# Performance work log

Measured on AMD Instinct MI355X. Metric: run time of the kernel, lower is better.

Reference implementation:

```python
import jax, jax.numpy as jnp
import numpy as np

NF = 128
NH = 512


def setup_inputs() -> dict:
    key = jax.random.key(0)
    k_x, k_wx, k_wh = jax.random.split(key, 3)
    B, T = 4096, 64
    x = jax.random.normal(k_x, (B, T, NF), dtype=jnp.float32)
    # GlorotUniform init: limit = sqrt(6 / (fan_in + fan_out))
    lim_x = float(np.sqrt(6.0 / (NF + NH)))
    lim_h = float(np.sqrt(6.0 / (NH + NH)))
    wx = jax.random.uniform(k_wx, (NF, NH), minval=-lim_x, maxval=lim_x, dtype=jnp.float32)
    wh = jax.random.uniform(k_wh, (NH, NH), minval=-lim_h, maxval=lim_h, dtype=jnp.float32)
    b = jnp.zeros((1, NH), dtype=jnp.float32)
    return {"x": x, "wx": wx, "wh": wh, "b": b}


def reference(x, wx, wh, b):
    # x: [B, T, nf] -> final hidden state [B, nh]
    B = x.shape[0]
    # Precompute input projections for all timesteps in one big GEMM: [T, B, nh]
    xz = jnp.einsum('btf,fh->tbh', x, wx) + b

    def step(h, xz_t):
        h = jnp.tanh(xz_t + h @ wh)
        return h, None

    h0 = jnp.zeros((B, wh.shape[0]), dtype=x.dtype)
    h_final, _ = jax.lax.scan(step, h0, xz)
    return h_final
```

## Files before the change

kernel.cpp:

```cpp
#include <hip/hip_runtime.h>
#include <math.h>


#define T_STEPS 64
#define NFD     128
#define NHD     512
#define BR      16
#define THREADS 1024
#define LDH     (NHD + 8)
#define LDX     (NFD + 8)

typedef _Float16 half8 __attribute__((ext_vector_type(8)));
typedef _Float16 half2v __attribute__((ext_vector_type(2)));
typedef float float4v __attribute__((ext_vector_type(4)));

__global__ __launch_bounds__(256) void rnn_prep(
    const float* __restrict__ wh, const float* __restrict__ wx,
    _Float16* __restrict__ whp_hi, _Float16* __restrict__ whp_lo,
    _Float16* __restrict__ wxp_hi, _Float16* __restrict__ wxp_lo)
{
    int idx = blockIdx.x * 256 + threadIdx.x;
    {
        int j  = idx & 7;
        int l  = (idx >> 3) & 63;
        int nt = (idx >> 9) & 3;
        int kb = (idx >> 11) & 15;
        int w  = idx >> 15;
        int k  = kb * 32 + (l >> 4) * 8 + j;
        int n  = w * 64 + nt * 16 + (l & 15);
        float v = wh[k * NHD + n];
        _Float16 hi = (_Float16)v;
        whp_hi[idx] = hi;
        whp_lo[idx] = (_Float16)(v - (float)hi);
    }
    if (idx < 65536) {
        int j  = idx & 7;
        int l  = (idx >> 3) & 63;
        int nt = (idx >> 9) & 3;
        int kb = (idx >> 11) & 3;
        int w  = idx >> 13;
        int k  = kb * 32 + (l >> 4) * 8 + j;
        int n  = w * 64 + nt * 16 + (l & 15);
        float v = wx[k * NHD + n];
        _Float16 hi = (_Float16)v;
        wxp_hi[idx] = hi;
        wxp_lo[idx] = (_Float16)(v - (float)hi);
    }
}

__device__ __forceinline__ float fast_tanh(float v) {
    float xc = fminf(fmaxf(v, -9.0f), 9.0f);
    float e  = __builtin_amdgcn_exp2f(xc * 2.8853900817779268f);
    return (e - 1.0f) * __builtin_amdgcn_rcpf(e + 1.0f);
}

__global__ __launch_bounds__(THREADS, 4) void rnn_mfma(
    const float* __restrict__ x,
    const float* __restrict__ bias,
    const _Float16* __restrict__ whp_hi, const _Float16* __restrict__ whp_lo,
    const _Float16* __restrict__ wxp_hi, const _Float16* __restrict__ wxp_lo,
    float* __restrict__ out)
{
    __shared__ _Float16 sh_hhi[BR * LDH];
    __shared__ _Float16 sh_hlo[BR * LDH];
    __shared__ _Float16 sh_xhi[BR * LDX];
    __shared__ _Float16 sh_xlo[BR * LDX];

    const int tid  = (int)threadIdx.x;
    const int lane = tid & 63;
    const int w    = tid >> 6;
    const int m    = lane & 15;
    const int quad = lane >> 4;
    const int row0 = (int)blockIdx.x * BR;

    for (int i = tid; i < BR * LDH; i += THREADS) {
        sh_hhi[i] = (_Float16)0.f;
        sh_hlo[i] = (_Float16)0.f;
    }

    float bv[2];
    #pragma unroll
    for (int nt = 0; nt < 2; ++nt) bv[nt] = bias[w * 32 + nt * 16 + m];

    const int xrow = tid >> 6;
    const int xcol = (tid & 63) * 2;
    const float* xptr = x + (size_t)(row0 + xrow) * (T_STEPS * NFD) + xcol;
    float2 px = *(const float2*)xptr;

    const half8* wxh = (const half8*)wxp_hi + (size_t)(w >> 1) * 1024 + (w & 1) * 128;
    const half8* wxl = (const half8*)wxp_lo + (size_t)(w >> 1) * 1024 + (w & 1) * 128;
    const half8* whh = (const half8*)whp_hi + (size_t)(w >> 1) * 4096 + (w & 1) * 128;
    const half8* whl = (const half8*)whp_lo + (size_t)(w >> 1) * 4096 + (w & 1) * 128;

    for (int t = 0; t < T_STEPS; ++t) {
        {
            half2v vh, vl;
            float xs[2] = {px.x, px.y};
            #pragma unroll
            for (int j = 0; j < 2; ++j) {
                _Float16 hi = (_Float16)xs[j];
                vh[j] = hi;
                vl[j] = (_Float16)(xs[j] - (float)hi);
            }
            *(half2v*)&sh_xhi[xrow * LDX + xcol] = vh;
            *(half2v*)&sh_xlo[xrow * LDX + xcol] = vl;
        }
        __syncthreads();

        if (t + 1 < T_STEPS) px = *(const float2*)(xptr + (t + 1) * NFD);

        float4v acc[2];
        #pragma unroll
        for (int nt = 0; nt < 2; ++nt) {
            acc[nt][0] = bv[nt]; acc[nt][1] = bv[nt];
            acc[nt][2] = bv[nt]; acc[nt][3] = bv[nt];
        }

        #pragma unroll
        for (int kb = 0; kb < 4; ++kb) {
            half8 ah = *(const half8*)&sh_xhi[m * LDX + kb * 32 + quad * 8];
            half8 al = *(const half8*)&sh_xlo[m * LDX + kb * 32 + quad * 8];
            half8 bh0 = wxh[kb * 256 + lane];
            half8 bh1 = wxh[kb * 256 + 64 + lane];
            half8 bl0 = wxl[kb * 256 + lane];
            half8 bl1 = wxl[kb * 256 + 64 + lane];
            acc[0] = __builtin_amdgcn_mfma_f32_16x16x32_f16(ah, bh0, acc[0], 0, 0, 0);
            acc[0] = __builtin_amdgcn_mfma_f32_16x16x32_f16(al, bh0, acc[0], 0, 0, 0);
            acc[0] = __builtin_amdgcn_mfma_f32_16x16x32_f16(ah, bl0, acc[0], 0, 0, 0);
            acc[1] = __builtin_amdgcn_mfma_f32_16x16x32_f16(ah, bh1, acc[1], 0, 0, 0);
            acc[1] = __builtin_amdgcn_mfma_f32_16x16x32_f16(al, bh1, acc[1], 0, 0, 0);
            acc[1] = __builtin_amdgcn_mfma_f32_16x16x32_f16(ah, bl1, acc[1], 0, 0, 0);
        }

        #pragma unroll 4
        for (int kb = 0; kb < 16; ++kb) {
            half8 ah = *(const half8*)&sh_hhi[m * LDH + kb * 32 + quad * 8];
            half8 al = *(const half8*)&sh_hlo[m * LDH + kb * 32 + quad * 8];
            half8 bh0 = whh[kb * 256 + lane];
            half8 bh1 = whh[kb * 256 + 64 + lane];
            half8 bl0 = whl[kb * 256 + lane];
            half8 bl1 = whl[kb * 256 + 64 + lane];
            acc[0] = __builtin_amdgcn_mfma_f32_16x16x32_f16(ah, bh0, acc[0], 0, 0, 0);
            acc[0] = __builtin_amdgcn_mfma_f32_16x16x32_f16(al, bh0, acc[0], 0, 0, 0);
            acc[0] = __builtin_amdgcn_mfma_f32_16x16x32_f16(ah, bl0, acc[0], 0, 0, 0);
            acc[1] = __builtin_amdgcn_mfma_f32_16x16x32_f16(ah, bh1, acc[1], 0, 0, 0);
            acc[1] = __builtin_amdgcn_mfma_f32_16x16x32_f16(al, bh1, acc[1], 0, 0, 0);
            acc[1] = __builtin_amdgcn_mfma_f32_16x16x32_f16(ah, bl1, acc[1], 0, 0, 0);
        }

        __syncthreads();

        if (t == T_STEPS - 1) {
            #pragma unroll
            for (int nt = 0; nt < 2; ++nt)
                #pragma unroll
                for (int r = 0; r < 4; ++r)
                    out[(size_t)(row0 + quad * 4 + r) * NHD + w * 32 + nt * 16 + m] =
                        fast_tanh(acc[nt][r]);
        } else {
            #pragma unroll
            for (int nt = 0; nt < 2; ++nt) {
                #pragma unroll
                for (int r = 0; r < 4; ++r) {
                    float v = fast_tanh(acc[nt][r]);
                    _Float16 hi = (_Float16)v;
                    int off = (quad * 4 + r) * LDH + w * 32 + nt * 16 + m;
                    sh_hhi[off] = hi;
                    sh_hlo[off] = (_Float16)(v - (float)hi);
                }
            }
        }
    }
}

extern "C" void kernel_launch(void* const* d_in, const int* in_sizes, int n_in,
                              void* d_out, int out_size, void* d_ws, size_t ws_size,
                              hipStream_t stream) {
    const float* x    = (const float*)d_in[0];
    const float* wx   = (const float*)d_in[1];
    const float* wh   = (const float*)d_in[2];
    const float* bias = (const float*)d_in[3];
    float* out = (float*)d_out;

    char* ws = (char*)d_ws;
    _Float16* whp_hi = (_Float16*)(ws);
    _Float16* whp_lo = (_Float16*)(ws + 524288);
    _Float16* wxp_hi = (_Float16*)(ws + 1048576);
    _Float16* wxp_lo = (_Float16*)(ws + 1048576 + 131072);

    rnn_prep<<<1024, 256, 0, stream>>>(wh, wx, whp_hi, whp_lo, wxp_hi, wxp_lo);

    const int B = in_sizes[0] / (T_STEPS * NFD);
    rnn_mfma<<<B / BR, THREADS, 0, stream>>>(x, bias, whp_hi, whp_lo, wxp_hi, wxp_lo, out);
}
```

Before: 843.5 us.

## Split hidden dimension across block pairs with global-memory h exchange and flags

Each 32-row batch tile is now handled by two cooperating blocks, each computing half of the hidden columns. The blocks swap their half of h through double-buffered global memory and spin on per-pair flags. The aim is to halve each block's Wh traffic per row and to overlap the own-half matmul with waiting for the partner. The risk is a deadlock if both partner blocks are not resident at the same time, since grid size is 256 blocks of 1024 threads. The per-step global round-trip and spin-wait also add latency, and a fallback path keeps the old kernel when the workspace is too small.

```diff
diff --git a/kernel.cpp b/kernel.cpp
--- a/kernel.cpp
+++ b/kernel.cpp
@@ -5,16 +5,238 @@
 #define T_STEPS 64
 #define NFD     128
 #define NHD     512
-#define BR      16
 #define THREADS 1024
-#define LDH     (NHD + 8)
 #define LDX     (NFD + 8)
 
 typedef _Float16 half8 __attribute__((ext_vector_type(8)));
+typedef _Float16 half4v __attribute__((ext_vector_type(4)));
 typedef _Float16 half2v __attribute__((ext_vector_type(2)));
 typedef float float4v __attribute__((ext_vector_type(4)));
 
+#define OFF_WHH   0u
+#define OFF_WHL   (512u<<10)
+#define OFF_WXH   (1024u<<10)
+#define OFF_WXL   (1152u<<10)
+#define OFF_FLAGS (1280u<<10)
+#define OFF_XH    (2048u<<10)
+#define OFF_XL    (10240u<<10)
+#define WS_NEED   (18432u<<10)
+
+__device__ __forceinline__ float fast_tanh(float v) {
+    float xc = fminf(fmaxf(v, -9.0f), 9.0f);
+    float e  = __builtin_amdgcn_exp2f(xc * 2.8853900817779268f);
+    return (e - 1.0f) * __builtin_amdgcn_rcpf(e + 1.0f);
+}
+
+
 __global__ __launch_bounds__(256) void rnn_prep(
+    const float* __restrict__ wh, const float* __restrict__ wx,
+    _Float16* __restrict__ whp_hi, _Float16* __restrict__ whp_lo,
+    _Float16* __restrict__ wxp_hi, _Float16* __restrict__ wxp_lo,
+    unsigned int* __restrict__ flags)
+{
+    int idx = blockIdx.x * 256 + threadIdx.x;
+    {
+        int j  = idx & 7;
+        int l  = (idx >> 3) & 63;
+        int ct = (idx >> 9) & 15;
+        int g  = (idx >> 13) & 15;
+        int c  = (idx >> 17) & 1;
+        int k  = g * 32 + (l >> 4) * 8 + j;
+        int n  = c * 256 + ct * 16 + (l & 15);
+        float v = wh[k * NHD + n];
+        _Float16 hi = (_Float16)v;
+        whp_hi[idx] = hi;
+        whp_lo[idx] = (_Float16)(v - (float)hi);
+    }
+    if (idx < 65536) {
+        int j  = idx & 7;
+        int l  = (idx >> 3) & 63;
+        int ct = (idx >> 9) & 15;
+        int kb = (idx >> 13) & 3;
+        int c  = (idx >> 15) & 1;
+        int k  = kb * 32 + (l >> 4) * 8 + j;
+        int n  = c * 256 + ct * 16 + (l & 15);
+        float v = wx[k * NHD + n];
+        _Float16 hi = (_Float16)v;
+        wxp_hi[idx] = hi;
+        wxp_lo[idx] = (_Float16)(v - (float)hi);
+    }
+    if (idx < 1024) flags[idx] = 0u;
+}
+
+__global__ __launch_bounds__(THREADS, 4) void rnn_mfma(
+    const float* __restrict__ x,
+    const float* __restrict__ bias,
+    const _Float16* __restrict__ whp_hi, const _Float16* __restrict__ whp_lo,
+    const _Float16* __restrict__ wxp_hi, const _Float16* __restrict__ wxp_lo,
+    _Float16* __restrict__ xchg_hi, _Float16* __restrict__ xchg_lo,
+    unsigned int* __restrict__ flags,
+    float* __restrict__ out)
+{
+    __shared__ _Float16 s_fh[8192];
+    __shared__ _Float16 s_fl[8192];
+    __shared__ _Float16 s_xh[32 * LDX];
+    __shared__ _Float16 s_xl[32 * LDX];
+
+    const int tid  = (int)threadIdx.x;
+    const int lane = tid & 63;
+    const int w    = tid >> 6;
+    const int m    = lane & 15;
+    const int quad = lane >> 4;
+
+    const int nrt = (int)gridDim.x >> 1;
+    const int c   = ((int)blockIdx.x >= nrt) ? 1 : 0;
+    const int rt  = (int)blockIdx.x - c * nrt;
+    const int row0 = rt * 32;
+
+    const int kblS = w >> 1;
+    const int qqS  = ((w & 1) * 2 + (m >> 3)) & 3;
+    const int jS   = m & 7;
+
+    const float bv = bias[c * 256 + w * 16 + m];
+
+    const int xrow = tid >> 5;
+    const int xcol = (tid & 31) * 4;
+    const float* xptr = x + (size_t)(row0 + xrow) * (T_STEPS * NFD) + xcol;
+    float4v px = *(const float4v*)xptr;
+
+    const half8* wxB_h = (const half8*)wxp_hi + (((size_t)c * 4) * 16 + w) * 64 + lane;
+    const half8* wxB_l = (const half8*)wxp_lo + (((size_t)c * 4) * 16 + w) * 64 + lane;
+    const half8* whB_h = (const half8*)whp_hi + (((size_t)c * 16) * 16 + w) * 64 + lane;
+    const half8* whB_l = (const half8*)whp_lo + (((size_t)c * 16) * 16 + w) * 64 + lane;
+    const int gOwn = c * 8;
+    const int gPrt = (1 - c) * 8;
+
+    unsigned int* flagMe = flags + (rt * 2 + c) * 2;
+    unsigned int* flagPr = flags + (rt * 2 + (c ^ 1)) * 2;
+
+    for (int t = 0; t < T_STEPS; ++t) {
+        {
+            half4v vh, vl;
+            float xs[4] = {px[0], px[1], px[2], px[3]};
+            #pragma unroll
+            for (int j = 0; j < 4; ++j) {
+                _Float16 hi = (_Float16)xs[j];
+                vh[j] = hi;
+                vl[j] = (_Float16)(xs[j] - (float)hi);
+            }
+            *(half4v*)&s_xh[xrow * LDX + xcol] = vh;
+            *(half4v*)&s_xl[xrow * LDX + xcol] = vl;
+        }
+        __syncthreads();
+
+        if (t + 1 < T_STEPS) px = *(const float4v*)(xptr + (t + 1) * NFD);
+
+        float4v acc[2];
+        #pragma unroll
+        for (int rb = 0; rb < 2; ++rb) {
+            acc[rb][0] = bv; acc[rb][1] = bv; acc[rb][2] = bv; acc[rb][3] = bv;
+        }
+
+        #pragma unroll
+        for (int kb = 0; kb < 4; ++kb) {
+            half8 bh = wxB_h[(size_t)kb * 1024];
+            half8 bl = wxB_l[(size_t)kb * 1024];
+            #pragma unroll
+            for (int rb = 0; rb < 2; ++rb) {
+                half8 ah = *(const half8*)&s_xh[(rb * 16 + m) * LDX + kb * 32 + quad * 8];
+                half8 al = *(const half8*)&s_xl[(rb * 16 + m) * LDX + kb * 32 + quad * 8];
+                acc[rb] = __builtin_amdgcn_mfma_f32_16x16x32_f16(ah, bh, acc[rb], 0, 0, 0);
+                acc[rb] = __builtin_amdgcn_mfma_f32_16x16x32_f16(al, bh, acc[rb], 0, 0, 0);
+                acc[rb] = __builtin_amdgcn_mfma_f32_16x16x32_f16(ah, bl, acc[rb], 0, 0, 0);
+            }
+        }
+
+        if (t > 0) {
+            #pragma unroll 4
+            for (int kbl = 0; kbl < 8; ++kbl) {
+                half8 bh = whB_h[(size_t)(gOwn + kbl) * 1024];
+                half8 bl = whB_l[(size_t)(gOwn + kbl) * 1024];
+                #pragma unroll
+                for (int rb = 0; rb < 2; ++rb) {
+                    half8 ah = *(const half8*)&s_fh[((rb * 8 + kbl) * 64 + lane) * 8];
+                    half8 al = *(const half8*)&s_fl[((rb * 8 + kbl) * 64 + lane) * 8];
+                    acc[rb] = __builtin_amdgcn_mfma_f32_16x16x32_f16(ah, bh, acc[rb], 0, 0, 0);
+                    acc[rb] = __builtin_amdgcn_mfma_f32_16x16x32_f16(al, bh, acc[rb], 0, 0, 0);
+                    acc[rb] = __builtin_amdgcn_mfma_f32_16x16x32_f16(ah, bl, acc[rb], 0, 0, 0);
+                }
+            }
+
+            if (tid == 0) {
+                unsigned int* fp = flagPr + ((t - 1) & 1);
+                while (__hip_atomic_load(fp, __ATOMIC_RELAXED, __HIP_MEMORY_SCOPE_AGENT) < (unsigned int)t) {}
+                (void)__hip_atomic_load(fp, __ATOMIC_ACQUIRE, __HIP_MEMORY_SCOPE_AGENT);
+            }
+            __syncthreads();
+
+            {
+                size_t slotR = ((size_t)((t - 1) & 1) * (nrt * 2) + rt * 2 + (c ^ 1)) * 1024;
+                #pragma unroll
+                for (int i = 0; i < 2; ++i) {
+                    int cid  = w * 2 + i;
+                    int comp = cid >> 4;
+                    int rbk  = cid & 15;
+                    const half8* src = (const half8*)(comp ? xchg_lo : xchg_hi) + slotR + rbk * 64 + lane;
+                    half8 v = *src;
+                    _Float16* dst = (comp ? s_fl : s_fh) + ((rbk * 64 + lane) * 8);
+                    *(half8*)dst = v;
+                }
+            }
+            __syncthreads();
+
+            #pragma unroll 4
+            for (int kbl = 0; kbl < 8; ++kbl) {
+                half8 bh = whB_h[(size_t)(gPrt + kbl) * 1024];
+                half8 bl = whB_l[(size_t)(gPrt + kbl) * 1024];
+                #pragma unroll
+                for (int rb = 0; rb < 2; ++rb) {
+                    half8 ah = *(const half8*)&s_fh[((rb * 8 + kbl) * 64 + lane) * 8];
+                    half8 al = *(const half8*)&s_fl[((rb * 8 + kbl) * 64 + lane) * 8];
+                    acc[rb] = __builtin_amdgcn_mfma_f32_16x16x32_f16(ah, bh, acc[rb], 0, 0, 0);
+                    acc[rb] = __builtin_amdgcn_mfma_f32_16x16x32_f16(al, bh, acc[rb], 0, 0, 0);
+                    acc[rb] = __builtin_amdgcn_mfma_f32_16x16x32_f16(ah, bl, acc[rb], 0, 0, 0);
+                }
+            }
+            __syncthreads();
+        }
+
+        if (t == T_STEPS - 1) {
+            #pragma unroll
+            for (int rb = 0; rb < 2; ++rb)
+                #pragma unroll
+                for (int r = 0; r < 4; ++r)
+                    out[(size_t)(row0 + rb * 16 + quad * 4 + r) * NHD + c * 256 + w * 16 + m] =
+                        fast_tanh(acc[rb][r]);
+        } else {
+            size_t slotW = ((size_t)(t & 1) * (nrt * 2) + rt * 2 + c) * 8192;
+            #pragma unroll
+            for (int rb = 0; rb < 2; ++rb) {
+                #pragma unroll
+                for (int r = 0; r < 4; ++r) {
+                    float v = fast_tanh(acc[rb][r]);
+                    _Float16 hi = (_Float16)v;
+                    _Float16 lo = (_Float16)(v - (float)hi);
+                    int fo = ((rb * 8 + kblS) * 64 + (qqS * 16 + quad * 4 + r)) * 8 + jS;
+                    s_fh[fo] = hi;
+                    s_fl[fo] = lo;
+                    xchg_hi[slotW + fo] = hi;
+                    xchg_lo[slotW + fo] = lo;
+                }
+            }
+            __syncthreads();
+            if (tid == 0) {
+                __hip_atomic_store(flagMe + (t & 1), (unsigned int)(t + 1),
+                                   __ATOMIC_RELEASE, __HIP_MEMORY_SCOPE_AGENT);
+            }
+        }
+    }
+}
+
+
+#define LDHF (NHD + 8)
+
+__global__ __launch_bounds__(256) void rnn_prep_fb(
     const float* __restrict__ wh, const float* __restrict__ wx,
     _Float16* __restrict__ whp_hi, _Float16* __restrict__ whp_lo,
     _Float16* __restrict__ wxp_hi, _Float16* __restrict__ wxp_lo)
@@ -48,32 +270,26 @@
     }
 }
 
-__device__ __forceinline__ float fast_tanh(float v) {
-    float xc = fminf(fmaxf(v, -9.0f), 9.0f);
-    float e  = __builtin_amdgcn_exp2f(xc * 2.8853900817779268f);
-    return (e - 1.0f) * __builtin_amdgcn_rcpf(e + 1.0f);
-}
-
-__global__ __launch_bounds__(THREADS, 4) void rnn_mfma(
+__global__ __launch_bounds__(1024, 4) void rnn_mfma_fb(
     const float* __restrict__ x,
     const float* __restrict__ bias,
     const _Float16* __restrict__ whp_hi, const _Float16* __restrict__ whp_lo,
     const _Float16* __restrict__ wxp_hi, const _Float16* __restrict__ wxp_lo,
     float* __restrict__ out)
 {
-    __shared__ _Float16 sh_hhi[BR * LDH];
-    __shared__ _Float16 sh_hlo[BR * LDH];
-    __shared__ _Float16 sh_xhi[BR * LDX];
-    __shared__ _Float16 sh_xlo[BR * LDX];
+    __shared__ _Float16 sh_hhi[16 * LDHF];
+    __shared__ _Float16 sh_hlo[16 * LDHF];
+    __shared__ _Float16 sh_xhi[16 * LDX];
+    __shared__ _Float16 sh_xlo[16 * LDX];
 
     const int tid  = (int)threadIdx.x;
     const int lane = tid & 63;
     const int w    = tid >> 6;
     const int m    = lane & 15;
     const int quad = lane >> 4;
-    const int row0 = (int)blockIdx.x * BR;
-
-    for (int i = tid; i < BR * LDH; i += THREADS) {
+    const int row0 = (int)blockIdx.x * 16;
+
+    for (int i = tid; i < 16 * LDHF; i += 1024) {
         sh_hhi[i] = (_Float16)0.f;
         sh_hlo[i] = (_Float16)0.f;
     }
@@ -134,8 +350,8 @@
 
         #pragma unroll 4
         for (int kb = 0; kb < 16; ++kb) {
-            half8 ah = *(const half8*)&sh_hhi[m * LDH + kb * 32 + quad * 8];
-            half8 al = *(const half8*)&sh_hlo[m * LDH + kb * 32 + quad * 8];
+            half8 ah = *(const half8*)&sh_hhi[m * LDHF + kb * 32 + quad * 8];
+            half8 al = *(const half8*)&sh_hlo[m * LDHF + kb * 32 + quad * 8];
             half8 bh0 = whh[kb * 256 + lane];
             half8 bh1 = whh[kb * 256 + 64 + lane];
             half8 bl0 = whl[kb * 256 + lane];
@@ -164,7 +380,7 @@
                 for (int r = 0; r < 4; ++r) {
                     float v = fast_tanh(acc[nt][r]);
                     _Float16 hi = (_Float16)v;
-                    int off = (quad * 4 + r) * LDH + w * 32 + nt * 16 + m;
+                    int off = (quad * 4 + r) * LDHF + w * 32 + nt * 16 + m;
                     sh_hhi[off] = hi;
                     sh_hlo[off] = (_Float16)(v - (float)hi);
                 }
@@ -172,6 +388,7 @@
         }
     }
 }
+
 
 extern "C" void kernel_launch(void* const* d_in, const int* in_sizes, int n_in,
                               void* d_out, int out_size, void* d_ws, size_t ws_size,
@@ -183,13 +400,22 @@
     float* out = (float*)d_out;
 
     char* ws = (char*)d_ws;
-    _Float16* whp_hi = (_Float16*)(ws);
-    _Float16* whp_lo = (_Float16*)(ws + 524288);
-    _Float16* wxp_hi = (_Float16*)(ws + 1048576);
-    _Float16* wxp_lo = (_Float16*)(ws + 1048576 + 131072);
-
-    rnn_prep<<<1024, 256, 0, stream>>>(wh, wx, whp_hi, whp_lo, wxp_hi, wxp_lo);
+    _Float16* whp_hi = (_Float16*)(ws + OFF_WHH);
+    _Float16* whp_lo = (_Float16*)(ws + OFF_WHL);
+    _Float16* wxp_hi = (_Float16*)(ws + OFF_WXH);
+    _Float16* wxp_lo = (_Float16*)(ws + OFF_WXL);
 
     const int B = in_sizes[0] / (T_STEPS * NFD);
-    rnn_mfma<<<B / BR, THREADS, 0, stream>>>(x, bias, whp_hi, whp_lo, wxp_hi, wxp_lo, out);
-}
+
+    if (ws_size >= (size_t)WS_NEED && (B % 32) == 0 && ((B / 32) % 8) == 0) {
+        unsigned int* flags = (unsigned int*)(ws + OFF_FLAGS);
+        _Float16* xchg_hi   = (_Float16*)(ws + OFF_XH);
+        _Float16* xchg_lo   = (_Float16*)(ws + OFF_XL);
+        rnn_prep<<<1024, 256, 0, stream>>>(wh, wx, whp_hi, whp_lo, wxp_hi, wxp_lo, flags);
+        rnn_mfma<<<(B / 32) * 2, THREADS, 0, stream>>>(
+            x, bias, whp_hi, whp_lo, wxp_hi, wxp_lo, xchg_hi, xchg_lo, flags, out);
+    } else {
+        rnn_prep_fb<<<1024, 256, 0, stream>>>(wh, wx, whp_hi, whp_lo, wxp_hi, wxp_lo);
+        rnn_mfma_fb<<<B / 16, 1024, 0, stream>>>(x, bias, whp_hi, whp_lo, wxp_hi, wxp_lo, out);
+    }
+}
```

Measured after the change: 1.422 ms. 68.6% more time.

## Keep packed weight fragments in registers and use fragment-major LDS layout

Applied to the files above, without the earlier changes.

The kernel now loads each wave's Wh and Wx hi/lo MFMA B-fragments into registers once, before the time loop, instead of re-reading them from global memory on every step. The hidden-state and input tiles in LDS switch to a fragment-major layout, so each lane reads its A-fragment with one contiguous 16-byte access instead of a padded row-major read. The aim is to cut repeated weight traffic and LDS bank conflicts. The cost is about 320 VGPRs of weights per thread, while a 1024-thread block only leaves around 128 per thread, so heavy scratch spilling is likely.

```diff
diff --git a/kernel.cpp b/kernel.cpp
--- a/kernel.cpp
+++ b/kernel.cpp
@@ -5,10 +5,7 @@
 #define T_STEPS 64
 #define NFD     128
 #define NHD     512
-#define BR      16
 #define THREADS 1024
-#define LDH     (NHD + 8)
-#define LDX     (NFD + 8)
 
 typedef _Float16 half8 __attribute__((ext_vector_type(8)));
 typedef _Float16 half2v __attribute__((ext_vector_type(2)));
@@ -61,36 +58,62 @@
     const _Float16* __restrict__ wxp_hi, const _Float16* __restrict__ wxp_lo,
     float* __restrict__ out)
 {
-    __shared__ _Float16 sh_hhi[BR * LDH];
-    __shared__ _Float16 sh_hlo[BR * LDH];
-    __shared__ _Float16 sh_xhi[BR * LDX];
-    __shared__ _Float16 sh_xlo[BR * LDX];
+    __shared__ _Float16 s_fh[16 * 64 * 8];
+    __shared__ _Float16 s_fl[16 * 64 * 8];
+    __shared__ _Float16 s_xh[4 * 64 * 8];
+    __shared__ _Float16 s_xl[4 * 64 * 8];
 
     const int tid  = (int)threadIdx.x;
     const int lane = tid & 63;
     const int w    = tid >> 6;
     const int m    = lane & 15;
     const int quad = lane >> 4;
-    const int row0 = (int)blockIdx.x * BR;
-
-    for (int i = tid; i < BR * LDH; i += THREADS) {
-        sh_hhi[i] = (_Float16)0.f;
-        sh_hlo[i] = (_Float16)0.f;
+    const int row0 = (int)blockIdx.x * 16;
+
+    for (int i = tid; i < 16 * 64 * 8; i += THREADS) {
+        s_fh[i] = (_Float16)0.f;
+        s_fl[i] = (_Float16)0.f;
     }
 
     float bv[2];
     #pragma unroll
     for (int nt = 0; nt < 2; ++nt) bv[nt] = bias[w * 32 + nt * 16 + m];
-
-    const int xrow = tid >> 6;
-    const int xcol = (tid & 63) * 2;
-    const float* xptr = x + (size_t)(row0 + xrow) * (T_STEPS * NFD) + xcol;
-    float2 px = *(const float2*)xptr;
 
     const half8* wxh = (const half8*)wxp_hi + (size_t)(w >> 1) * 1024 + (w & 1) * 128;
     const half8* wxl = (const half8*)wxp_lo + (size_t)(w >> 1) * 1024 + (w & 1) * 128;
     const half8* whh = (const half8*)whp_hi + (size_t)(w >> 1) * 4096 + (w & 1) * 128;
     const half8* whl = (const half8*)whp_lo + (size_t)(w >> 1) * 4096 + (w & 1) * 128;
+
+    half8 WHh[16][2], WHl[16][2];
+    half8 WXh[4][2],  WXl[4][2];
+    #pragma unroll
+    for (int kb = 0; kb < 16; ++kb) {
+        #pragma unroll
+        for (int nt = 0; nt < 2; ++nt) {
+            WHh[kb][nt] = whh[kb * 256 + nt * 64 + lane];
+            WHl[kb][nt] = whl[kb * 256 + nt * 64 + lane];
+        }
+    }
+    #pragma unroll
+    for (int kb = 0; kb < 4; ++kb) {
+        #pragma unroll
+        for (int nt = 0; nt < 2; ++nt) {
+            WXh[kb][nt] = wxh[kb * 256 + nt * 64 + lane];
+            WXl[kb][nt] = wxl[kb * 256 + nt * 64 + lane];
+        }
+    }
+
+    const int xrow  = tid >> 6;
+    const int xcol  = (tid & 63) * 2;
+    const int xkb   = xcol >> 5;
+    const int xkk   = xcol & 31;
+    const int xoff  = (xkb * 64 + (xrow + 16 * (xkk >> 3))) * 8 + (xkk & 7);
+    const float* xptr = x + (size_t)(row0 + xrow) * (T_STEPS * NFD) + xcol;
+    float2 px = *(const float2*)xptr;
+
+    const int eBase = w * 64 * 8 + (m & 7);
+    const int eQ    = quad * 4;
+    const int eHiM  = 16 * (m >> 3);
 
     for (int t = 0; t < T_STEPS; ++t) {
         {
@@ -102,8 +125,8 @@
                 vh[j] = hi;
                 vl[j] = (_Float16)(xs[j] - (float)hi);
             }
-            *(half2v*)&sh_xhi[xrow * LDX + xcol] = vh;
-            *(half2v*)&sh_xlo[xrow * LDX + xcol] = vl;
+            *(half2v*)&s_xh[xoff] = vh;
+            *(half2v*)&s_xl[xoff] = vl;
         }
         __syncthreads();
 
@@ -118,34 +141,26 @@
 
         #pragma unroll
         for (int kb = 0; kb < 4; ++kb) {
-            half8 ah = *(const half8*)&sh_xhi[m * LDX + kb * 32 + quad * 8];
-            half8 al = *(const half8*)&sh_xlo[m * LDX + kb * 32 + quad * 8];
-            half8 bh0 = wxh[kb * 256 + lane];
-            half8 bh1 = wxh[kb * 256 + 64 + lane];
-            half8 bl0 = wxl[kb * 256 + lane];
-            half8 bl1 = wxl[kb * 256 + 64 + lane];
-            acc[0] = __builtin_amdgcn_mfma_f32_16x16x32_f16(ah, bh0, acc[0], 0, 0, 0);
-            acc[0] = __builtin_amdgcn_mfma_f32_16x16x32_f16(al, bh0, acc[0], 0, 0, 0);
-            acc[0] = __builtin_amdgcn_mfma_f32_16x16x32_f16(ah, bl0, acc[0], 0, 0, 0);
-            acc[1] = __builtin_amdgcn_mfma_f32_16x16x32_f16(ah, bh1, acc[1], 0, 0, 0);
-            acc[1] = __builtin_amdgcn_mfma_f32_16x16x32_f16(al, bh1, acc[1], 0, 0, 0);
-            acc[1] = __builtin_amdgcn_mfma_f32_16x16x32_f16(ah, bl1, acc[1], 0, 0, 0);
-        }
-
-        #pragma unroll 4
+            half8 ah = *(const half8*)&s_xh[(kb * 64 + lane) * 8];
+            half8 al = *(const half8*)&s_xl[(kb * 64 + lane) * 8];
+            acc[0] = __builtin_amdgcn_mfma_f32_16x16x32_f16(ah, WXh[kb][0], acc[0], 0, 0, 0);
+            acc[0] = __builtin_amdgcn_mfma_f32_16x16x32_f16(al, WXh[kb][0], acc[0], 0, 0, 0);
+            acc[0] = __builtin_amdgcn_mfma_f32_16x16x32_f16(ah, WXl[kb][0], acc[0], 0, 0, 0);
+            acc[1] = __builtin_amdgcn_mfma_f32_16x16x32_f16(ah, WXh[kb][1], acc[1], 0, 0, 0);
+            acc[1] = __builtin_amdgcn_mfma_f32_16x16x32_f16(al, WXh[kb][1], acc[1], 0, 0, 0);
+            acc[1] = __builtin_amdgcn_mfma_f32_16x16x32_f16(ah, WXl[kb][1], acc[1], 0, 0, 0);
+        }
+
+        #pragma unroll
         for (int kb = 0; kb < 16; ++kb) {
-            half8 ah = *(const half8*)&sh_hhi[m * LDH + kb * 32 + quad * 8];
-            half8 al = *(const half8*)&sh_hlo[m * LDH + kb * 32 + quad * 8];
-            half8 bh0 = whh[kb * 256 + lane];
-            half8 bh1 = whh[kb * 256 + 64 + lane];
-            half8 bl0 = whl[kb * 256 + lane];
-            half8 bl1 = whl[kb * 256 + 64 + lane];
-            acc[0] = __builtin_amdgcn_mfma_f32_16x16x32_f16(ah, bh0, acc[0], 0, 0, 0);
-            acc[0] = __builtin_amdgcn_mfma_f32_16x16x32_f16(al, bh0, acc[0], 0, 0, 0);
-            acc[0] = __builtin_amdgcn_mfma_f32_16x16x32_f16(ah, bl0, acc[0], 0, 0, 0);
-            acc[1] = __builtin_amdgcn_mfma_f32_16x16x32_f16(ah, bh1, acc[1], 0, 0, 0);
-            acc[1] = __builtin_amdgcn_mfma_f32_16x16x32_f16(al, bh1, acc[1], 0, 0, 0);
-            acc[1] = __builtin_amdgcn_mfma_f32_16x16x32_f16(ah, bl1, acc[1], 0, 0, 0);
+            half8 ah = *(const half8*)&s_fh[(kb * 64 + lane) * 8];
+            half8 al = *(const half8*)&s_fl[(kb * 64 + lane) * 8];
+            acc[0] = __builtin_amdgcn_mfma_f32_16x16x32_f16(ah, WHh[kb][0], acc[0], 0, 0, 0);
+            acc[0] = __builtin_amdgcn_mfma_f32_16x16x32_f16(al, WHh[kb][0], acc[0], 0, 0, 0);
+            acc[0] = __builtin_amdgcn_mfma_f32_16x16x32_f16(ah, WHl[kb][0], acc[0], 0, 0, 0);
+            acc[1] = __builtin_amdgcn_mfma_f32_16x16x32_f16(ah, WHh[kb][1], acc[1], 0, 0, 0);
+            acc[1] = __builtin_amdgcn_mfma_f32_16x16x32_f16(al, WHh[kb][1], acc[1], 0, 0, 0);
+            acc[1] = __builtin_amdgcn_mfma_f32_16x16x32_f16(ah, WHl[kb][1], acc[1], 0, 0, 0);
         }
 
         __syncthreads();
@@ -164,9 +179,9 @@
                 for (int r = 0; r < 4; ++r) {
                     float v = fast_tanh(acc[nt][r]);
                     _Float16 hi = (_Float16)v;
-                    int off = (quad * 4 + r) * LDH + w * 32 + nt * 16 + m;
-                    sh_hhi[off] = hi;
-                    sh_hlo[off] = (_Float16)(v - (float)hi);
+                    int fo = eBase + (eQ + r + 16 * (nt * 2) + eHiM) * 8;
+                    s_fh[fo] = hi;
+                    s_fl[fo] = (_Float16)(v - (float)hi);
                 }
             }
         }
@@ -191,5 +206,5 @@
     rnn_prep<<<1024, 256, 0, stream>>>(wh, wx, whp_hi, whp_lo, wxp_hi, wxp_lo);
 
     const int B = in_sizes[0] / (T_STEPS * NFD);
-    rnn_mfma<<<B / BR, THREADS, 0, stream>>>(x, bias, whp_hi, whp_lo, wxp_hi, wxp_lo, out);
-}
+    rnn_mfma<<<B / 16, THREADS, 0, stream>>>(x, bias, whp_hi, whp_lo, wxp_hi, wxp_lo, out);
+}
```

After: 2.838 ms. 3.36x slower.

## Double rows per block and store LDS operands in MFMA fragment order

Applied to the files above, without the earlier changes.

Each block now processes 32 batch rows as two 16-row MFMA tiles, so every wh/wx fragment loaded from global memory feeds twice as many MFMAs. The hidden-state and input staging buffers in LDS are rearranged into per-lane fragment order, which makes A-operand reads contiguous half8 loads and removes the padded row layout. x loads are widened to float4. The cost is half as many blocks (128 for B=4096), which may leave many CUs idle, and more accumulator registers per thread.

```diff
diff --git a/kernel.cpp b/kernel.cpp
--- a/kernel.cpp
+++ b/kernel.cpp
@@ -5,13 +5,11 @@
 #define T_STEPS 64
 #define NFD     128
 #define NHD     512
-#define BR      16
+#define BR      32
 #define THREADS 1024
-#define LDH     (NHD + 8)
-#define LDX     (NFD + 8)
 
 typedef _Float16 half8 __attribute__((ext_vector_type(8)));
-typedef _Float16 half2v __attribute__((ext_vector_type(2)));
+typedef _Float16 half4v __attribute__((ext_vector_type(4)));
 typedef float float4v __attribute__((ext_vector_type(4)));
 
 __global__ __launch_bounds__(256) void rnn_prep(
@@ -61,10 +59,10 @@
     const _Float16* __restrict__ wxp_hi, const _Float16* __restrict__ wxp_lo,
     float* __restrict__ out)
 {
-    __shared__ _Float16 sh_hhi[BR * LDH];
-    __shared__ _Float16 sh_hlo[BR * LDH];
-    __shared__ _Float16 sh_xhi[BR * LDX];
-    __shared__ _Float16 sh_xlo[BR * LDX];
+    __shared__ _Float16 s_fh[2 * 16 * 64 * 8];
+    __shared__ _Float16 s_fl[2 * 16 * 64 * 8];
+    __shared__ _Float16 s_xh[2 * 4 * 64 * 8];
+    __shared__ _Float16 s_xl[2 * 4 * 64 * 8];
 
     const int tid  = (int)threadIdx.x;
     const int lane = tid & 63;
@@ -73,100 +71,132 @@
     const int quad = lane >> 4;
     const int row0 = (int)blockIdx.x * BR;
 
-    for (int i = tid; i < BR * LDH; i += THREADS) {
-        sh_hhi[i] = (_Float16)0.f;
-        sh_hlo[i] = (_Float16)0.f;
+    for (int i = tid; i < 2 * 16 * 64 * 8; i += THREADS) {
+        s_fh[i] = (_Float16)0.f;
+        s_fl[i] = (_Float16)0.f;
     }
 
     float bv[2];
     #pragma unroll
     for (int nt = 0; nt < 2; ++nt) bv[nt] = bias[w * 32 + nt * 16 + m];
-
-    const int xrow = tid >> 6;
-    const int xcol = (tid & 63) * 2;
-    const float* xptr = x + (size_t)(row0 + xrow) * (T_STEPS * NFD) + xcol;
-    float2 px = *(const float2*)xptr;
 
     const half8* wxh = (const half8*)wxp_hi + (size_t)(w >> 1) * 1024 + (w & 1) * 128;
     const half8* wxl = (const half8*)wxp_lo + (size_t)(w >> 1) * 1024 + (w & 1) * 128;
     const half8* whh = (const half8*)whp_hi + (size_t)(w >> 1) * 4096 + (w & 1) * 128;
     const half8* whl = (const half8*)whp_lo + (size_t)(w >> 1) * 4096 + (w & 1) * 128;
 
+    const int xrow = tid >> 5;
+    const int xcol = (tid & 31) * 4;
+    const int xrb  = xrow >> 4;
+    const int xrr  = xrow & 15;
+    const int xkb  = xcol >> 5;
+    const int xkk  = xcol & 31;
+    const int xoff = ((xrb * 4 + xkb) * 64 + (xrr + 16 * (xkk >> 3))) * 8 + (xkk & 7);
+    const float* xptr = x + (size_t)(row0 + xrow) * (T_STEPS * NFD) + xcol;
+    float4v px = *(const float4v*)xptr;
+
+    const int eJ   = m & 7;
+    const int eQ   = quad * 4;
+    const int eHiM = 16 * (m >> 3);
+
     for (int t = 0; t < T_STEPS; ++t) {
         {
-            half2v vh, vl;
-            float xs[2] = {px.x, px.y};
-            #pragma unroll
-            for (int j = 0; j < 2; ++j) {
+            half4v vh, vl;
+            float xs[4] = {px[0], px[1], px[2], px[3]};
+            #pragma unroll
+            for (int j = 0; j < 4; ++j) {
                 _Float16 hi = (_Float16)xs[j];
                 vh[j] = hi;
                 vl[j] = (_Float16)(xs[j] - (float)hi);
             }
-            *(half2v*)&sh_xhi[xrow * LDX + xcol] = vh;
-            *(half2v*)&sh_xlo[xrow * LDX + xcol] = vl;
+            *(half4v*)&s_xh[xoff] = vh;
+            *(half4v*)&s_xl[xoff] = vl;
         }
         __syncthreads();
 
-        if (t + 1 < T_STEPS) px = *(const float2*)(xptr + (t + 1) * NFD);
-
-        float4v acc[2];
+        if (t + 1 < T_STEPS) px = *(const float4v*)(xptr + (t + 1) * NFD);
+
+        float4v acc[2][2];
         #pragma unroll
-        for (int nt = 0; nt < 2; ++nt) {
-            acc[nt][0] = bv[nt]; acc[nt][1] = bv[nt];
-            acc[nt][2] = bv[nt]; acc[nt][3] = bv[nt];
-        }
+        for (int rb = 0; rb < 2; ++rb)
+            #pragma unroll
+            for (int nt = 0; nt < 2; ++nt) {
+                acc[rb][nt][0] = bv[nt]; acc[rb][nt][1] = bv[nt];
+                acc[rb][nt][2] = bv[nt]; acc[rb][nt][3] = bv[nt];
+            }
 
         #pragma unroll
         for (int kb = 0; kb < 4; ++kb) {
-            half8 ah = *(const half8*)&sh_xhi[m * LDX + kb * 32 + quad * 8];
-            half8 al = *(const half8*)&sh_xlo[m * LDX + kb * 32 + quad * 8];
+            half8 a0h = *(const half8*)&s_xh[((    kb) * 64 + lane) * 8];
+            half8 a0l = *(const half8*)&s_xl[((    kb) * 64 + lane) * 8];
+            half8 a1h = *(const half8*)&s_xh[((4 + kb) * 64 + lane) * 8];
+            half8 a1l = *(const half8*)&s_xl[((4 + kb) * 64 + lane) * 8];
             half8 bh0 = wxh[kb * 256 + lane];
             half8 bh1 = wxh[kb * 256 + 64 + lane];
             half8 bl0 = wxl[kb * 256 + lane];
             half8 bl1 = wxl[kb * 256 + 64 + lane];
-            acc[0] = __builtin_amdgcn_mfma_f32_16x16x32_f16(ah, bh0, acc[0], 0, 0, 0);
-            acc[0] = __builtin_amdgcn_mfma_f32_16x16x32_f16(al, bh0, acc[0], 0, 0, 0);
-            acc[0] = __builtin_amdgcn_mfma_f32_16x16x32_f16(ah, bl0, acc[0], 0, 0, 0);
-            acc[1] = __builtin_amdgcn_mfma_f32_16x16x32_f16(ah, bh1, acc[1], 0, 0, 0);
-            acc[1] = __builtin_amdgcn_mfma_f32_16x16x32_f16(al, bh1, acc[1], 0, 0, 0);
-            acc[1] = __builtin_amdgcn_mfma_f32_16x16x32_f16(ah, bl1, acc[1], 0, 0, 0);
+            acc[0][0] = __builtin_amdgcn_mfma_f32_16x16x32_f16(a0h, bh0, acc[0][0], 0, 0, 0);
+            acc[0][0] = __builtin_amdgcn_mfma_f32_16x16x32_f16(a0l, bh0, acc[0][0], 0, 0, 0);
+            acc[0][0] = __builtin_amdgcn_mfma_f32_16x16x32_f16(a0h, bl0, acc[0][0], 0, 0, 0);
+            acc[0][1] = __builtin_amdgcn_mfma_f32_16x16x32_f16(a0h, bh1, acc[0][1], 0, 0, 0);
+            acc[0][1] = __builtin_amdgcn_mfma_f32_16x16x32_f16(a0l, bh1, acc[0][1], 0, 0, 0);
+            acc[0][1] = __builtin_amdgcn_mfma_f32_16x16x32_f16(a0h, bl1, acc[0][1], 0, 0, 0);
+            acc[1][0] = __builtin_amdgcn_mfma_f32_16x16x32_f16(a1h, bh0, acc[1][0], 0, 0, 0);
+            acc[1][0] = __builtin_amdgcn_mfma_f32_16x16x32_f16(a1l, bh0, acc[1][0], 0, 0, 0);
+            acc[1][0] = __builtin_amdgcn_mfma_f32_16x16x32_f16(a1h, bl0, acc[1][0], 0, 0, 0);
+            acc[1][1] = __builtin_amdgcn_mfma_f32_16x16x32_f16(a1h, bh1, acc[1][1], 0, 0, 0);
+            acc[1][1] = __builtin_amdgcn_mfma_f32_16x16x32_f16(a1l, bh1, acc[1][1], 0, 0, 0);
+            acc[1][1] = __builtin_amdgcn_mfma_f32_16x16x32_f16(a1h, bl1, acc[1][1], 0, 0, 0);
         }
 
         #pragma unroll 4
         for (int kb = 0; kb < 16; ++kb) {
-            half8 ah = *(const half8*)&sh_hhi[m * LDH + kb * 32 + quad * 8];
-            half8 al = *(const half8*)&sh_hlo[m * LDH + kb * 32 + quad * 8];
+            half8 a0h = *(const half8*)&s_fh[((     kb) * 64 + lane) * 8];
+            half8 a0l = *(const half8*)&s_fl[((     kb) * 64 + lane) * 8];
+            half8 a1h = *(const half8*)&s_fh[((16 + kb) * 64 + lane) * 8];
+            half8 a1l = *(const half8*)&s_fl[((16 + kb) * 64 + lane) * 8];
             half8 bh0 = whh[kb * 256 + lane];
             half8 bh1 = whh[kb * 256 + 64 + lane];
             half8 bl0 = whl[kb * 256 + lane];
             half8 bl1 = whl[kb * 256 + 64 + lane];
-            acc[0] = __builtin_amdgcn_mfma_f32_16x16x32_f16(ah, bh0, acc[0], 0, 0, 0);
-            acc[0] = __builtin_amdgcn_mfma_f32_16x16x32_f16(al, bh0, acc[0], 0, 0, 0);
-            acc[0] = __builtin_amdgcn_mfma_f32_16x16x32_f16(ah, bl0, acc[0], 0, 0, 0);
-            acc[1] = __builtin_amdgcn_mfma_f32_16x16x32_f16(ah, bh1, acc[1], 0, 0, 0);
-            acc[1] = __builtin_amdgcn_mfma_f32_16x16x32_f16(al, bh1, acc[1], 0, 0, 0);
-            acc[1] = __builtin_amdgcn_mfma_f32_16x16x32_f16(ah, bl1, acc[1], 0, 0, 0);
+            acc[0][0] = __builtin_amdgcn_mfma_f32_16x16x32_f16(a0h, bh0, acc[0][0], 0, 0, 0);
+            acc[0][0] = __builtin_amdgcn_mfma_f32_16x16x32_f16(a0l, bh0, acc[0][0], 0, 0, 0);
+            acc[0][0] = __builtin_amdgcn_mfma_f32_16x16x32_f16(a0h, bl0, acc[0][0], 0, 0, 0);
+            acc[0][1] = __builtin_amdgcn_mfma_f32_16x16x32_f16(a0h, bh1, acc[0][1], 0, 0, 0);
+            acc[0][1] = __builtin_amdgcn_mfma_f32_16x16x32_f16(a0l, bh1, acc[0][1], 0, 0, 0);
+            acc[0][1] = __builtin_amdgcn_mfma_f32_16x16x32_f16(a0h, bl1, acc[0][1], 0, 0, 0);
+            acc[1][0] = __builtin_amdgcn_mfma_f32_16x16x32_f16(a1h, bh0, acc[1][0], 0, 0, 0);
+            acc[1][0] = __builtin_amdgcn_mfma_f32_16x16x32_f16(a1l, bh0, acc[1][0], 0, 0, 0);
+            acc[1][0] = __builtin_amdgcn_mfma_f32_16x16x32_f16(a1h, bl0, acc[1][0], 0, 0, 0);
+            acc[1][1] = __builtin_amdgcn_mfma_f32_16x16x32_f16(a1h, bh1, acc[1][1], 0, 0, 0);
+            acc[1][1] = __builtin_amdgcn_mfma_f32_16x16x32_f16(a1l, bh1, acc[1][1], 0, 0, 0);
+            acc[1][1] = __builtin_amdgcn_mfma_f32_16x16x32_f16(a1h, bl1, acc[1][1], 0, 0, 0);
         }
 
         __syncthreads();
 
         if (t == T_STEPS - 1) {
             #pragma unroll
-            for (int nt = 0; nt < 2; ++nt)
+            for (int rb = 0; rb < 2; ++rb)
                 #pragma unroll
-                for (int r = 0; r < 4; ++r)
-                    out[(size_t)(row0 + quad * 4 + r) * NHD + w * 32 + nt * 16 + m] =
-                        fast_tanh(acc[nt][r]);
+                for (int nt = 0; nt < 2; ++nt)
+                    #pragma unroll
+                    for (int r = 0; r < 4; ++r)
+                        out[(size_t)(row0 + rb * 16 + quad * 4 + r) * NHD + w * 32 + nt * 16 + m] =
+                            fast_tanh(acc[rb][nt][r]);
         } else {
             #pragma unroll
-            for (int nt = 0; nt < 2; ++nt) {
+            for (int rb = 0; rb < 2; ++rb) {
                 #pragma unroll
-                for (int r = 0; r < 4; ++r) {
-                    float v = fast_tanh(acc[nt][r]);
-                    _Float16 hi = (_Float16)v;
-                    int off = (quad * 4 + r) * LDH + w * 32 + nt * 16 + m;
-                    sh_hhi[off] = hi;
-                    sh_hlo[off] = (_Float16)(v - (float)hi);
+                for (int nt = 0; nt < 2; ++nt) {
+                    #pragma unroll
+                    for (int r = 0; r < 4; ++r) {
+                        float v = fast_tanh(acc[rb][nt][r]);
+                        _Float16 hi = (_Float16)v;
+                        int fo = ((rb * 16 + w) * 64 + (eQ + r + 16 * (nt * 2) + eHiM)) * 8 + eJ;
+                        s_fh[fo] = hi;
+                        s_fl[fo] = (_Float16)(v - (float)hi);
+                    }
                 }
             }
         }
```

Measured after the change: 1.018 ms. +20.7%, slower.
